# Optimization experiments

Hardware: AMD Instinct MI355X
Metric: run time of the kernel (lower is better)

Reference implementation:

```python
import jax, jax.numpy as jnp
import numpy as np

EPS = 1e-6      # vnn EPS used in norms / leaky-relu denominators
BN_EPS = 1e-5   # torch BatchNorm eps
K = 20          # args.n_knn


def vnlin(W, x):
    # VNLinear: apply (O,C) weight over channel axis 1 of x (B,C,3,...)
    return jnp.moveaxis(jnp.tensordot(W, x, axes=((1,), (1,))), 0, 1)


def vn_bn(x):
    # VNBatchNorm (training-mode batch stats, affine = identity init):
    # normalizes the per-vector norms, rescales vectors accordingly.
    norm = jnp.sqrt(jnp.sum(x * x, axis=2)) + EPS        # (B,C,...)
    axes = (0,) + tuple(range(2, norm.ndim))             # per-channel stats
    mean = jnp.mean(norm, axis=axes, keepdims=True)
    var = jnp.var(norm, axis=axes, keepdims=True)
    norm_bn = (norm - mean) / jnp.sqrt(var + BN_EPS)
    return x / jnp.expand_dims(norm, 2) * jnp.expand_dims(norm_bn, 2)


def vn_lrelu(Wf, Wd, x):
    # VNLinearLeakyReLU with negative_slope=0 (as constructed in this module)
    p = vn_bn(vnlin(Wf, x))
    d = vnlin(Wd, x)
    dot = jnp.sum(p * d, axis=2, keepdims=True)
    dsq = jnp.sum(d * d, axis=2, keepdims=True)
    return jnp.where(dot >= 0, p, p - (dot / (dsq + EPS)) * d)


def vn_maxpool(Wd, x):
    # VNMaxPool: pool over last axis, picking per (b,c) the vector maximizing <x,d>
    d = vnlin(Wd, x)
    dot = jnp.sum(x * d, axis=2, keepdims=True)          # (B,C,1,...)
    idx = jnp.argmax(dot, axis=-1)                       # (B,C,1,...)
    idx = jnp.broadcast_to(idx[..., None], x.shape[:-1] + (1,))
    return jnp.take_along_axis(x, idx, axis=-1)[..., 0]


def graph_feature_cross(x, k):
    # x: (B,3,N) -> (B, 3ch, 3vec, N, k); channels = [nbr-x, x, cross(nbr,x)]
    xx = jnp.sum(x * x, axis=1)                          # (B,N)
    inner = jnp.einsum('bdi,bdj->bij', x, x)             # (B,N,N)
    pd = 2.0 * inner - xx[:, :, None] - xx[:, None, :]   # = -||xi-xj||^2
    idx = jax.lax.top_k(pd, k)[1]                        # (B,N,k) nearest
    pts = jnp.swapaxes(x, 1, 2)                          # (B,N,3)
    nb = jax.vmap(lambda p, i: p[i])(pts, idx)           # (B,N,k,3) gather
    c = jnp.broadcast_to(pts[:, :, None, :], nb.shape)   # center repeated
    cross = jnp.cross(nb, c)
    feat = jnp.stack([nb - c, c, cross], axis=3)         # (B,N,k,3,3)
    return jnp.transpose(feat, (0, 3, 4, 1, 2))


_W_SPECS = {
    'pos_Wf': (21, 3), 'pos_Wd': (21, 3), 'pool_Wd': (21, 21),
    'c1_Wf': (21, 21), 'c1_Wd': (21, 21),
    'st1_Wf': (21, 21), 'st1_Wd': (21, 21),
    'st2_Wf': (42, 21), 'st2_Wd': (42, 21),
    'st3_Wf': (341, 42), 'st3_Wd': (341, 42),
    'st_pool_Wd': (341, 341),
    'stf1_Wf': (170, 341), 'stf1_Wd': (170, 341),
    'stf2_Wf': (85, 170), 'stf2_Wd': (85, 170),
    'stf3_W': (21, 85),
    'c2_Wf': (42, 42), 'c2_Wd': (42, 42),
    'c3_W': (341, 42),
    'std1_Wf': (341, 682), 'std1_Wd': (341, 682),
    'std2_Wf': (170, 341), 'std2_Wd': (170, 341),
    'std_lin': (3, 170),
}


def setup_inputs() -> dict:
    key = jax.random.key(0)
    ks = iter(jax.random.split(key, 32))
    inp = {'x': jax.random.normal(next(ks), (8, 3, 4096), dtype=jnp.float32)}
    for name, (o, i) in _W_SPECS.items():
        inp[name] = jax.random.normal(next(ks), (o, i), dtype=jnp.float32) / np.sqrt(i).astype(np.float32)
    return inp


def _forward(x, pos_Wf, pos_Wd, pool_Wd, c1_Wf, c1_Wd, st1_Wf, st1_Wd, st2_Wf, st2_Wd,
             st3_Wf, st3_Wd, st_pool_Wd, stf1_Wf, stf1_Wd, stf2_Wf, stf2_Wd, stf3_W,
             c2_Wf, c2_Wd, c3_W, std1_Wf, std1_Wd, std2_Wf, std2_Wd, std_lin):
    B, D, N = x.shape
    feat = graph_feature_cross(x, K)                     # (B,3,3,N,k)
    h = vn_lrelu(pos_Wf, pos_Wd, feat)                   # (B,21,3,N,k)
    h = vn_maxpool(pool_Wd, h)                           # (B,21,3,N) pool over k
    h = vn_lrelu(c1_Wf, c1_Wd, h)                        # (B,21,3,N)
    # STNkd feature transform
    s = vn_lrelu(st1_Wf, st1_Wd, h)                      # (B,21,3,N)
    s = vn_lrelu(st2_Wf, st2_Wd, s)                      # (B,42,3,N)
    s = vn_lrelu(st3_Wf, st3_Wd, s)                      # (B,341,3,N)
    s = vn_maxpool(st_pool_Wd, s)                        # (B,341,3) pool over N
    s = vn_lrelu(stf1_Wf, stf1_Wd, s)                    # (B,170,3)
    s = vn_lrelu(stf2_Wf, stf2_Wd, s)                    # (B,85,3)
    s = vnlin(stf3_W, s)                                 # (B,21,3)
    s = jnp.broadcast_to(s[..., None], h.shape)          # repeat over N
    h = jnp.concatenate([h, s], axis=1)                  # (B,42,3,N)
    h = vn_lrelu(c2_Wf, c2_Wd, h)                        # (B,42,3,N)
    h = vn_bn(vnlin(c3_W, h))                            # (B,341,3,N)
    h_mean = jnp.broadcast_to(jnp.mean(h, axis=-1, keepdims=True), h.shape)
    h = jnp.concatenate([h, h_mean], axis=1)             # (B,682,3,N)
    # VNStdFeature (normalize_frame=False)
    z0 = vn_lrelu(std1_Wf, std1_Wd, h)                   # (B,341,3,N)
    z0 = vn_lrelu(std2_Wf, std2_Wd, z0)                  # (B,170,3,N)
    z0 = vnlin(std_lin, z0)                              # (B,3,3,N)
    h_std = jnp.einsum('bijm,bjkm->bikm', h, z0)         # (B,682,3,N)
    out = jnp.max(h_std.reshape(B, -1, N), axis=-1)      # (B,2046)
    return out, z0


def reference(x, pos_Wf, pos_Wd, pool_Wd, c1_Wf, c1_Wd, st1_Wf, st1_Wd, st2_Wf, st2_Wd,
              st3_Wf, st3_Wd, st_pool_Wd, stf1_Wf, stf1_Wd, stf2_Wf, stf2_Wd, stf3_W,
              c2_Wf, c2_Wd, c3_W, std1_Wf, std1_Wd, std2_Wf, std2_Wd, std_lin):
    return _forward(x, pos_Wf, pos_Wd, pool_Wd, c1_Wf, c1_Wd, st1_Wf, st1_Wd, st2_Wf,
                    st2_Wd, st3_Wf, st3_Wd, st_pool_Wd, stf1_Wf, stf1_Wd, stf2_Wf,
                    stf2_Wd, stf3_W, c2_Wf, c2_Wd, c3_W, std1_Wf, std1_Wd, std2_Wf,
                    std2_Wd, std_lin)
```

## Files before the change

kernel.cpp:

```cpp
#include <hip/hip_runtime.h>
#include <cstdint>
#include <cstddef>


typedef unsigned short u16;
using bh8  = __attribute__((ext_vector_type(8))) short;
using f32x4 = __attribute__((ext_vector_type(4))) float;

__device__ __forceinline__ float b2f(u16 v) {
  return __uint_as_float(((unsigned)v) << 16);
}
__device__ __forceinline__ u16 f2b(float f) {
  unsigned u = __float_as_uint(f);
  u += 0x7FFFu + ((u >> 16) & 1u);
  return (u16)(u >> 16);
}

__device__ __forceinline__ void st4(float* p, size_t i, float a, float b, float c, float d) {
  float4 v; v.x = a; v.y = b; v.z = c; v.w = d; *(float4*)(p + i) = v;
}

#define FMA4(A, S, V) { A.x += (S)*(V).x; A.y += (S)*(V).y; A.z += (S)*(V).z; A.w += (S)*(V).w; }

__device__ __forceinline__ unsigned long long packKey(float v, int n) {
// ... 58 lines not shown
  int lane = tid & 63, wave = tid >> 6;
  #pragma unroll
  for (int c = 0; c < 21; ++c) {
    float w0 = wf[c * 3], w1 = wf[c * 3 + 1], w2 = wf[c * 3 + 2];
    float p0 = w0 * e00 + w1 * c0 + w2 * e20;
    float p1 = w0 * e01 + w1 * c1 + w2 * e21;
    float p2 = w0 * e02 + w1 * c2 + w2 * e22;
    float nr = sqrtf(p0 * p0 + p1 * p1 + p2 * p2) + 1e-6f;
    float u1 = nr, u2 = nr * nr;
    #pragma unroll
    for (int off = 32; off; off >>= 1) { u1 += __shfl_down(u1, off); u2 += __shfl_down(u2, off); }
    if (lane == 0) { part[wave][c] = u1; part[wave][21 + c] = u2; }
  }
  __syncthreads();
  if (tid < 42) {
    float t = part[0][tid] + part[1][tid] + part[2][tid] + part[3][tid];
    if (tid < 21) atomicAdd(&statSum[tid], t);
    else atomicAdd(&statSq[tid - 21], t);
  }
}

__global__ __launch_bounds__(64) void pos_apply(const float* __restrict__ x,
                                                const int* __restrict__ idx,
                                                const float* __restrict__ Wf,
                                                const float* __restrict__ Wd,
                                                const float* __restrict__ Wpool,
                                                const float* __restrict__ statMean,
                                                const float* __restrict__ statIstd,
                                                float* __restrict__ h0, int N) {
  __shared__ float wpool[441];
  __shared__ float hbuf[64];
  int tid = threadIdx.x;
  for (int l = tid; l < 441; l += 64) wpool[l] = Wpool[l];
  int b = blockIdx.y, n = blockIdx.x;
  bool act = tid < 63;
  int c = act ? tid / 3 : 0;
  int v = act ? tid - c * 3 : 0;
  const float* xb = x + (size_t)b * 3 * N;
  float c0 = xb[n], c1 = xb[N + n], c2 = xb[2 * (size_t)N + n];
  float wf0 = 0, wf1 = 0, wf2 = 0, wd0 = 0, wd1 = 0, wd2 = 0, mn = 0, is = 1.f;
  if (act) {
    wf0 = Wf[c * 3]; wf1 = Wf[c * 3 + 1]; wf2 = Wf[c * 3 + 2];
    wd0 = Wd[c * 3]; wd1 = Wd[c * 3 + 1]; wd2 = Wd[c * 3 + 2];
    mn = statMean[c]; is = statIstd[c];
  }
  __syncthreads();
  float best = -3.4e38f, bh = 0.f;
  const int* idxRow = idx + ((size_t)b * N + n) * 20;
  for (int kk = 0; kk < 20; ++kk) {
    int j = idxRow[kk];
    float a0 = xb[j], a1 = xb[N + j], a2 = xb[2 * (size_t)N + j];
    float av  = (v == 0) ? a0 : ((v == 1) ? a1 : a2);
    float cv  = (v == 0) ? c0 : ((v == 1) ? c1 : c2);
    float a1v = (v == 0) ? a1 : ((v == 1) ? a2 : a0);
    float a2v = (v == 0) ? a2 : ((v == 1) ? a0 : a1);
    float c1v = (v == 0) ? c1 : ((v == 1) ? c2 : c0);
    float c2v = (v == 0) ? c2 : ((v == 1) ? c0 : c1);
    float e0 = av - cv;
    float e1 = cv;
    float e2 = a1v * c2v - a2v * c1v;
    float p = wf0 * e0 + wf1 * e1 + wf2 * e2;
    float d = wd0 * e0 + wd1 * e1 + wd2 * e2;
    int base = c * 3;
    float pp = p * p;
    float n2 = __shfl(pp, base) + __shfl(pp, base + 1) + __shfl(pp, base + 2);
    float nr = sqrtf(n2) + 1e-6f;
    float sc = ((nr - mn) * is) / nr;
    float pb = p * sc;
    float pd2 = pb * d, dd = d * d;
    float dot = __shfl(pd2, base) + __shfl(pd2, base + 1) + __shfl(pd2, base + 2);
    float dsq = __shfl(dd, base) + __shfl(dd, base + 1) + __shfl(dd, base + 2);
    float h = (dot >= 0.f) ? pb : pb - (dot / (dsq + 1e-6f)) * d;
    hbuf[tid] = act ? h : 0.f;
    __syncthreads();
    float d2 = 0.f;
    #pragma unroll 7
    for (int cc = 0; cc < 21; ++cc) d2 += wpool[c * 21 + cc] * hbuf[cc * 3 + v];
    float hd = h * d2;
    float dotp = __shfl(hd, base) + __shfl(hd, base + 1) + __shfl(hd, base + 2);
    if (act && dotp > best) { best = dotp; bh = h; }
    __syncthreads();
  }
  if (act) h0[(((size_t)b * 32 + c) * 3 + v) * N + n] = bh;
}

__global__ void zero_padch(float* __restrict__ p, int Cfrom, int Cpad, int N) {
  size_t t = (size_t)blockIdx.x * 256 + threadIdx.x;
  size_t per = (size_t)(Cpad - Cfrom) * 3 * N;
  if (t >= 8 * per) return;
  int b = (int)(t / per);
  size_t r = t - (size_t)b * per;
  p[(((size_t)b * Cpad + Cfrom) * 3) * N + r] = 0.f;
}

template<int MODE, int CPT>
__global__ __launch_bounds__(256) void gemm_db(
    const float* __restrict__ Wp, const float* __restrict__ Xp,
    float* __restrict__ Yp,
    float* __restrict__ statSum, float* __restrict__ statSq,
    const float* __restrict__ statMean, const float* __restrict__ statIstd,
    int Cout, int CpadY, int Kpad, int N) {
  __shared__ float Xs[2][16][3][64];
  __shared__ float Wfs[2][16 * CPT][16];
  const int tid = threadIdx.x;
  const int tx = tid & 15, ty = tid >> 4;
  const int lane = tid & 63, w = tid >> 6;
  const int b = blockIdx.z;
  const int n0 = blockIdx.x * 64;
  const int co0 = blockIdx.y * (16 * CPT);
  const float* Xb = Xp + (size_t)b * Kpad * 3 * N;

  auto stage = [&](int k0, int buf) {
    #pragma unroll
    for (int l0 = 0; l0 < 12; ++l0) {
      int q = l0 * 4 + w;
      int vv = q % 3, kk = q / 3;
      const float* g = Xb + ((size_t)(k0 + kk) * 3 + vv) * N + n0 + lane;
      __builtin_amdgcn_global_load_lds(
          (const __attribute__((address_space(1))) float*)g,
          (__attribute__((address_space(3))) float*)&Xs[buf][kk][vv][0], 4, 0, 0);
    }
    #pragma unroll
    for (int c = 0; c < CPT; ++c) {
      const float* g = Wp + (size_t)(co0 + w * 4 + (lane >> 4) + 16 * c) * Kpad + k0 + (lane & 15);
      __builtin_amdgcn_global_load_lds(
          (const __attribute__((address_space(1))) float*)g,
          (__attribute__((address_space(3))) float*)&Wfs[buf][w * 4 + 16 * c][0], 4, 0, 0);
    }
  };

  float4 acc[CPT][3];
  #pragma unroll
  for (int c = 0; c < CPT; ++c)
    #pragma unroll
    for (int v = 0; v < 3; ++v) acc[c][v] = {0.f, 0.f, 0.f, 0.f};

  stage(0, 0);
  __syncthreads();
  const int KT = Kpad / 16;
  for (int kt = 0; kt < KT; ++kt) {
    int buf = kt & 1;
    if (kt + 1 < KT) stage((kt + 1) * 16, buf ^ 1);
    #pragma unroll
    for (int kk = 0; kk < 16; ++kk) {
      float4 x0 = *(const float4*)&Xs[buf][kk][0][tx * 4];
      float4 x1 = *(const float4*)&Xs[buf][kk][1][tx * 4];
      float4 x2 = *(const float4*)&Xs[buf][kk][2][tx * 4];
      #pragma unroll
      for (int c = 0; c < CPT; ++c) {
        float wv = Wfs[buf][ty + 16 * c][kk];
        FMA4(acc[c][0], wv, x0); FMA4(acc[c][1], wv, x1); FMA4(acc[c][2], wv, x2);
      }
    }
    __syncthreads();
  }

  #pragma unroll
  for (int c = 0; c < CPT; ++c) {
    int co = co0 + ty + 16 * c;
    if (co >= CpadY) continue;
    const float* a0 = (const float*)&acc[c][0];
    const float* a1 = (const float*)&acc[c][1];
    const float* a2 = (const float*)&acc[c][2];
    size_t yb = ((size_t)b * CpadY + co) * 3 * N + n0 + tx * 4;
    if constexpr (MODE == 5) {
      float s1 = 0.f, s2 = 0.f;
      #pragma unroll
      for (int j = 0; j < 4; ++j) {
        float nr = sqrtf(a0[j]*a0[j] + a1[j]*a1[j] + a2[j]*a2[j]) + 1e-6f;
        s1 += nr; s2 += nr * nr;
      }
      st4(Yp, yb,                 a0[0], a0[1], a0[2], a0[3]);
      st4(Yp, yb + N,             a1[0], a1[1], a1[2], a1[3]);
      st4(Yp, yb + 2 * (size_t)N, a2[0], a2[1], a2[2], a2[3]);
      #pragma unroll
      for (int off = 8; off; off >>= 1) { s1 += __shfl_down(s1, off); s2 += __shfl_down(s2, off); }
      if (tx == 0 && co < Cout) { atomicAdd(&statSum[co], s1); atomicAdd(&statSq[co], s2); }
    } else {
      if (co < Cout) {
        float mn = statMean[co], is = statIstd[co];
        float4 P0 = *(const float4*)&Yp[yb];
        float4 P1 = *(const float4*)&Yp[yb + N];
        float4 P2 = *(const float4*)&Yp[yb + 2 * (size_t)N];
        float pr[3][4] = {{P0.x,P0.y,P0.z,P0.w},{P1.x,P1.y,P1.z,P1.w},{P2.x,P2.y,P2.z,P2.w}};
        float o_[3][4];
        #pragma unroll
        for (int j = 0; j < 4; ++j) {
          float q0 = pr[0][j], q1 = pr[1][j], q2 = pr[2][j];
          float e0 = a0[j], e1 = a1[j], e2 = a2[j];
          float nr = sqrtf(q0*q0 + q1*q1 + q2*q2) + 1e-6f;
          float sc = ((nr - mn) * is) / nr;
          q0 *= sc; q1 *= sc; q2 *= sc;
          float dot = q0*e0 + q1*e1 + q2*e2;
          if (dot < 0.f) {
            float dsq = e0*e0 + e1*e1 + e2*e2;
            float t = dot / (dsq + 1e-6f);
            q0 -= t*e0; q1 -= t*e1; q2 -= t*e2;
          }
          o_[0][j] = q0; o_[1][j] = q1; o_[2][j] = q2;
        }
        st4(Yp, yb,                 o_[0][0], o_[0][1], o_[0][2], o_[0][3]);
        st4(Yp, yb + N,             o_[1][0], o_[1][1], o_[1][2], o_[1][3]);
        st4(Yp, yb + 2 * (size_t)N, o_[2][0], o_[2][1], o_[2][2], o_[2][3]);
      } else {
        st4(Yp, yb, 0.f, 0.f, 0.f, 0.f);
        st4(Yp, yb + N, 0.f, 0.f, 0.f, 0.f);
        st4(Yp, yb + 2 * (size_t)N, 0.f, 0.f, 0.f, 0.f);
      }
    }
  }
}

__global__ __launch_bounds__(256) void gemm_pool_db(
    const float* __restrict__ Wp, const float* __restrict__ Xp,
    unsigned long long* __restrict__ poolPart, int Cout, int N) {
  constexpr int KP = 352, CPT = 4;
  __shared__ float Xs[2][16][3][64];
  __shared__ float Wfs[2][16 * CPT][16];
  const int tid = threadIdx.x;
  const int tx = tid & 15, ty = tid >> 4;
  const int lane = tid & 63, w = tid >> 6;
  const int b = blockIdx.z;
  const int n0 = blockIdx.x * 64;
  const int co0 = blockIdx.y * (16 * CPT);
  const float* Xb = Xp + (size_t)b * KP * 3 * N;

  auto stage = [&](int k0, int buf) {
    #pragma unroll
    for (int l0 = 0; l0 < 12; ++l0) {
      int q = l0 * 4 + w;
      int vv = q % 3, kk = q / 3;
      const float* g = Xb + ((size_t)(k0 + kk) * 3 + vv) * N + n0 + lane;
      __builtin_amdgcn_global_load_lds(
          (const __attribute__((address_space(1))) float*)g,
          (__attribute__((address_space(3))) float*)&Xs[buf][kk][vv][0], 4, 0, 0);
    }
    #pragma unroll
    for (int c = 0; c < CPT; ++c) {
      const float* g = Wp + (size_t)(co0 + w * 4 + (lane >> 4) + 16 * c) * KP + k0 + (lane & 15);
      __builtin_amdgcn_global_load_lds(
          (const __attribute__((address_space(1))) float*)g,
          (__attribute__((address_space(3))) float*)&Wfs[buf][w * 4 + 16 * c][0], 4, 0, 0);
    }
  };

  float4 acc[CPT][3];
  #pragma unroll
  for (int c = 0; c < CPT; ++c)
    #pragma unroll
    for (int v = 0; v < 3; ++v) acc[c][v] = {0.f, 0.f, 0.f, 0.f};

  stage(0, 0);
  __syncthreads();
  constexpr int KT = KP / 16;
  for (int kt = 0; kt < KT; ++kt) {
    int buf = kt & 1;
    if (kt + 1 < KT) stage((kt + 1) * 16, buf ^ 1);
    #pragma unroll
    for (int kk = 0; kk < 16; ++kk) {
      float4 x0 = *(const float4*)&Xs[buf][kk][0][tx * 4];
      float4 x1 = *(const float4*)&Xs[buf][kk][1][tx * 4];
      float4 x2 = *(const float4*)&Xs[buf][kk][2][tx * 4];
      #pragma unroll
      for (int c = 0; c < CPT; ++c) {
        float wv = Wfs[buf][ty + 16 * c][kk];
        FMA4(acc[c][0], wv, x0); FMA4(acc[c][1], wv, x1); FMA4(acc[c][2], wv, x2);
      }
    }
    __syncthreads();
  }

  #pragma unroll
  for (int c = 0; c < CPT; ++c) {
    int co = co0 + ty + 16 * c;
    unsigned long long key = 0;
    if (co < Cout) {
      const float* av0 = (const float*)&acc[c][0];
      const float* av1 = (const float*)&acc[c][1];
      const float* av2 = (const float*)&acc[c][2];
      size_t xb2 = ((size_t)co * 3) * N + n0 + tx * 4;
      #pragma unroll
      for (int j = 0; j < 4; ++j) {
        float X0 = Xb[xb2 + j];
        float X1 = Xb[xb2 + N + j];
        float X2 = Xb[xb2 + 2 * (size_t)N + j];
        float dot = X0 * av0[j] + X1 * av1[j] + X2 * av2[j];
        unsigned long long k2 = packKey(dot, n0 + tx * 4 + j);
        if (k2 > key) key = k2;
      }
    }
    #pragma unroll
    for (int off = 8; off; off >>= 1) {
      unsigned long long o = __shfl_down(key, off);
      if (o > key) key = o;
    }
    if (tx == 0 && co < Cout) poolPart[((size_t)b * Cout + co) * 64 + blockIdx.x] = key;
  }
}

// ... 35 lines not shown
  for (int s = 0; s < NS; ++s) {
    int cb = co0 + s * 16 + quad * 4;
    if constexpr (MODE == 0) {
      #pragma unroll
      for (int r = 0; r < 4; ++r) {
        int co = cb + r;
        if (co < Cout) {
          size_t zb = (((size_t)b * Cout + co) * 3) * N + n;
          Zout[zb] = acc[s][0][r];
          Zout[zb + N] = acc[s][1][r];
          Zout[zb + 2 * (size_t)N] = acc[s][2][r];
        }
      }
    } else if constexpr (MODE == 1) {
      if (cb < Cpad) {
        float q[3][4];
        #pragma unroll
        for (int r = 0; r < 4; ++r) {
          int co = cb + r;
          float b0 = 0, b1 = 0, b2 = 0;
          if (biasP != nullptr && co < Cout) {
            size_t bi = ((size_t)b * Cout + co) * 3;
            b0 = biasP[bi]; b1 = biasP[bi + 1]; b2 = biasP[bi + 2];
          }
          float q0 = acc[s][0][r] + b0, q1 = acc[s][1][r] + b1, q2 = acc[s][2][r] + b2;
          if (co >= Cout) { q0 = 0.f; q1 = 0.f; q2 = 0.f; }
          q[0][r] = q0; q[1][r] = q1; q[2][r] = q2;
          float nr = sqrtf(q0*q0 + q1*q1 + q2*q2) + 1e-6f;
          float s1 = nr, s2 = nr * nr;
          #pragma unroll
          for (int off = 1; off < 16; off <<= 1) { s1 += __shfl_xor(s1, off); s2 += __shfl_xor(s2, off); }
          if (l16 == 0 && co < Cout) { atomicAdd(&statSum[co], s1); atomicAdd(&statSq[co], s2); }
        }
        #pragma unroll
        for (int v = 0; v < 3; ++v) {
          u16 ob[4];
          ob[0] = f2b(q[v][0]); ob[1] = f2b(q[v][1]); ob[2] = f2b(q[v][2]); ob[3] = f2b(q[v][3]);
          *(ushort4*)(Pb + ((size_t)v * N + n) * Cpad + cb) = *(ushort4*)ob;
        }
      }
    } else {
      if (cb < Cpad) {
        u16 pa[3][4];
        #pragma unroll
        for (int v = 0; v < 3; ++v)
          *(ushort4*)pa[v] = *(const ushort4*)(Pb + ((size_t)v * N + n) * Cpad + cb);
        float o[3][4];
        #pragma unroll
        for (int r = 0; r < 4; ++r) {
          int co = cb + r;
          float r0 = 0.f, r1 = 0.f, r2 = 0.f;
          if (co < Cout) {
            float p0 = b2f(pa[0][r]), p1 = b2f(pa[1][r]), p2 = b2f(pa[2][r]);
            float d0 = acc[s][0][r], d1 = acc[s][1][r], d2 = acc[s][2][r];
            if (biasD != nullptr) {
              size_t bi = ((size_t)b * Cout + co) * 3;
              d0 += biasD[bi]; d1 += biasD[bi + 1]; d2 += biasD[bi + 2];
            }
            float mn = statMean[co], is = statIstd[co];
            float nr = sqrtf(p0*p0 + p1*p1 + p2*p2) + 1e-6f;
            float sc = ((nr - mn) * is) / nr;
            float q0 = p0 * sc, q1 = p1 * sc, q2 = p2 * sc;
            float dot = q0*d0 + q1*d1 + q2*d2;
            if (dot < 0.f) {
              float dsq = d0*d0 + d1*d1 + d2*d2;
              float t = dot / (dsq + 1e-6f);
              q0 -= t*d0; q1 -= t*d1; q2 -= t*d2;
            }
            r0 = q0; r1 = q1; r2 = q2;
          }
          o[0][r] = r0; o[1][r] = r1; o[2][r] = r2;
        }
        #pragma unroll
        for (int v = 0; v < 3; ++v) {
          u16 ob[4];
          ob[0] = f2b(o[v][0]); ob[1] = f2b(o[v][1]); ob[2] = f2b(o[v][2]); ob[3] = f2b(o[v][3]);
          *(ushort4*)(Pb + ((size_t)v * N + n) * Cpad + cb) = *(ushort4*)ob;
        }
      }
    }
  }
}

__global__ void w_to_bf16(const float* __restrict__ W, u16* __restrict__ Wp,
                          int Cout, int Cin, int wstride, int CoutPad, int Kpad) {
  int t = blockIdx.x * 256 + threadIdx.x;
  if (t >= CoutPad * Kpad) return;
  int co = t / Kpad, ci = t - co * Kpad;
  Wp[t] = (co < Cout && ci < Cin) ? f2b(W[(size_t)co * wstride + ci]) : (u16)0;
}

__global__ void w_to_f32pad(const float* __restrict__ W, float* __restrict__ Wp,
                            int Cout, int Cin, int wstride, int CoutPad, int Kpad) {
  int t = blockIdx.x * 256 + threadIdx.x;
  if (t >= CoutPad * Kpad) return;
  int co = t / Kpad, ci = t - co * Kpad;
  Wp[t] = (co < Cout && ci < Cin) ? W[(size_t)co * wstride + ci] : 0.f;
}

__global__ void zero_kernel(float* p, int n) {
  int t = blockIdx.x * 256 + threadIdx.x;
  if (t < n) p[t] = 0.f;
}

__global__ void finalize_kernel(float* __restrict__ sum, float* __restrict__ sq,
                                float* __restrict__ mean, float* __restrict__ istd,
                                int C, float invCount) {
  int c = blockIdx.x * 256 + threadIdx.x;
  if (c < C) {
    float m = sum[c] * invCount;
    float v = sq[c] * invCount - m * m;
    if (v < 0.f) v = 0.f;
    mean[c] = m;
    istd[c] = 1.f / sqrtf(v + 1e-5f);
  }
  if (c < 512) { sum[c] = 0.f; sq[c] = 0.f; }
}

__global__ __launch_bounds__(64) void pool_reduce(const unsigned long long* __restrict__ part,
                                                  const float* __restrict__ s3,
                                                  float* __restrict__ pooled, int N) {
  int co = blockIdx.x, b = blockIdx.y, lane = threadIdx.x;
  unsigned long long key = part[((size_t)b * 341 + co) * 64 + lane];
  #pragma unroll
  for (int off = 32; off; off >>= 1) {
    unsigned long long o = __shfl_down(key, off);
    if (o > key) key = o;
  }
  if (lane == 0) {
    int n = (int)(0xFFFFFFFFu - (unsigned)(key & 0xFFFFFFFFull));
    size_t base = ((size_t)b * 352 + co) * 3;
    size_t obase = ((size_t)b * 341 + co) * 3;
    pooled[obase + 0] = s3[(base + 0) * N + n];
    pooled[obase + 1] = s3[(base + 1) * N + n];
    pooled[obase + 2] = s3[(base + 2) * N + n];
  }
}

__global__ __launch_bounds__(64) void stf_lrelu(const float* __restrict__ Wf,
                                                const float* __restrict__ Wd,
                                                const float* __restrict__ X,
                                                float* __restrict__ Y, int Cin, int Cout) {
  __shared__ float P[24], D[24], NORM[8], SC[8], DOT[8], DSQ[8], MS[2];
  int co = blockIdx.x, tid = threadIdx.x;
  if (tid < 48) {
    int l = tid < 24 ? tid : tid - 24;
    int b = l / 3, v = l - b * 3;
    const float* W = (tid < 24 ? Wf : Wd) + (size_t)co * Cin;
    const float* xb = X + ((size_t)b * Cin) * 3 + v;
    float acc = 0.f;
    for (int ci = 0; ci < Cin; ++ci) acc += W[ci] * xb[ci * 3];
    if (tid < 24) P[l] = acc; else D[l] = acc;
  }
  __syncthreads();
  if (tid < 8) NORM[tid] = sqrtf(P[tid*3]*P[tid*3] + P[tid*3+1]*P[tid*3+1] + P[tid*3+2]*P[tid*3+2]) + 1e-6f;
  __syncthreads();
  if (tid == 0) {
    float m = 0.f;
    for (int b2 = 0; b2 < 8; ++b2) m += NORM[b2];
    m *= 0.125f;
    float var = 0.f;
    for (int b2 = 0; b2 < 8; ++b2) { float dd = NORM[b2] - m; var += dd * dd; }
    var *= 0.125f;
    MS[0] = m; MS[1] = 1.f / sqrtf(var + 1e-5f);
  }
  __syncthreads();
  if (tid < 8) {
    float sc = ((NORM[tid] - MS[0]) * MS[1]) / NORM[tid];
    float dot = 0.f, dsq = 0.f;
    for (int v = 0; v < 3; ++v) {
      float pb = P[tid*3+v] * sc; float dv = D[tid*3+v];
      dot += pb * dv; dsq += dv * dv;
    }
    SC[tid] = sc; DOT[tid] = dot; DSQ[tid] = dsq;
  }
  __syncthreads();
  if (tid < 24) {
    int b = tid / 3;
    float pb = P[tid] * SC[b];
    float o = (DOT[b] >= 0.f) ? pb : pb - (DOT[b] / (DSQ[b] + 1e-6f)) * D[tid];
    Y[((size_t)b * Cout + co) * 3 + (tid - b * 3)] = o;
  }
}

__global__ void vnlin_small(const float* __restrict__ W, const float* __restrict__ X,
                            float* __restrict__ Y, int Cin, int Cout) {
  int t = blockIdx.x * 256 + threadIdx.x;
  if (t >= 8 * Cout * 3) return;
  int v = t % 3, r = t / 3;
  int co = r % Cout, b = r / Cout;
  float acc = 0.f;
  for (int ci = 0; ci < Cin; ++ci) acc += W[(size_t)co * Cin + ci] * X[((size_t)b * Cin + ci) * 3 + v];
  Y[t] = acc;
}

__global__ __launch_bounds__(256) void concat_tt(const float* __restrict__ h1,
                                                 const float* __restrict__ sfin,
                                                 u16* __restrict__ s2bb, int N) {
  __shared__ u16 tile[64][66];
  int b = blockIdx.z, v = blockIdx.y, n0 = blockIdx.x * 64;
  int tn = threadIdx.x & 63, tc = threadIdx.x >> 6;
  for (int c = tc; c < 64; c += 4) {
    u16 val = 0;
    if (c < 21) val = f2b(h1[(((size_t)b * 32 + c) * 3 + v) * N + n0 + tn]);
    else if (c < 42) val = f2b(sfin[((size_t)b * 21 + (c - 21)) * 3 + v]);
    tile[c][tn] = val;
  }
  __syncthreads();
  u16* dst = s2bb + (((size_t)b * 3 + v) * N + n0) * 64;
  for (int n = tc; n < 64; n += 4)
    dst[(size_t)n * 64 + tn] = tile[tn][n];
}

__global__ __launch_bounds__(384) void bn_apply_mean(u16* __restrict__ H,
    const float* __restrict__ sMean, const float* __restrict__ sIstd,
    float* __restrict__ HmAcc, int N) {
  int c = threadIdx.x;
  if (c >= 341) return;
  int b = blockIdx.y, nt = blockIdx.x;
  float mn = sMean[c], is = sIstd[c];
  float a0 = 0.f, a1 = 0.f, a2 = 0.f;
  size_t base = (size_t)b * 3 * N * 352;
  for (int n = nt * 64; n < nt * 64 + 64; ++n) {
    size_t i0 = base + ((size_t)0 * N + n) * 352 + c;
    size_t i1 = base + ((size_t)1 * N + n) * 352 + c;
    size_t i2 = base + ((size_t)2 * N + n) * 352 + c;
    float p0 = b2f(H[i0]), p1 = b2f(H[i1]), p2 = b2f(H[i2]);
    float nr = sqrtf(p0*p0 + p1*p1 + p2*p2) + 1e-6f;
    float sc = ((nr - mn) * is) / nr;
    p0 *= sc; p1 *= sc; p2 *= sc;
    H[i0] = f2b(p0); H[i1] = f2b(p1); H[i2] = f2b(p2);
    a0 += p0; a1 += p1; a2 += p2;
  }
  size_t hb = ((size_t)b * 341 + c) * 3;
  atomicAdd(&HmAcc[hb], a0); atomicAdd(&HmAcc[hb + 1], a1); atomicAdd(&HmAcc[hb + 2], a2);
}

__global__ void hm_finalize(float* Hm, float invN) {
  int t = blockIdx.x * 256 + threadIdx.x;
  if (t < 8 * 341 * 3) Hm[t] *= invN;
}

__global__ void bias_kernel(const float* __restrict__ Wf, const float* __restrict__ Wd,
                            const float* __restrict__ Hm,
                            float* __restrict__ biasP, float* __restrict__ biasD) {
  int t = blockIdx.x * 256 + threadIdx.x;
  if (t >= 8 * 341 * 3) return;
  int v = t % 3, r = t / 3;
  int co = r % 341, b = r / 341;
  const float* hm = Hm + (size_t)b * 1023 + v;
  float ap = 0.f, ad = 0.f;
  for (int j = 0; j < 341; ++j) {
    float h = hm[j * 3];
    ap += Wf[(size_t)co * 682 + 341 + j] * h;
    ad += Wd[(size_t)co * 682 + 341 + j] * h;
  }
  biasP[t] = ap; biasD[t] = ad;
}

__global__ __launch_bounds__(256) void final_max_part(const u16* __restrict__ H,
    const float* __restrict__ Hm, const float* __restrict__ z0,
    float* __restrict__ part, int N, int NT) {
  __shared__ float red[3][4][64];
  int b = blockIdx.z, nt = blockIdx.y;
  int il = threadIdx.x & 63, nsub = threadIdx.x >> 6;
  int i = blockIdx.x * 64 + il;
  bool valid = i < 682, lo = i < 341;
  float c0 = 0, c1 = 0, c2 = 0;
  if (valid && !lo) {
    size_t hb = ((size_t)b * 341 + (i - 341)) * 3;
    c0 = Hm[hb]; c1 = Hm[hb + 1]; c2 = Hm[hb + 2];
  }
  const float* zb = z0 + (size_t)b * 9 * N;
  const u16* Hb = H + (size_t)b * 3 * N * 352;
  float m0 = -3.4e38f, m1 = -3.4e38f, m2 = -3.4e38f;
  int ii = lo ? i : 0;
  int chunk = N / NT, nBeg = nt * chunk;
  for (int n = nBeg + nsub; n < nBeg + chunk; n += 4) {
    float a0, a1, a2;
    if (lo) {
      a0 = b2f(Hb[((size_t)0 * N + n) * 352 + ii]);
      a1 = b2f(Hb[((size_t)1 * N + n) * 352 + ii]);
      a2 = b2f(Hb[((size_t)2 * N + n) * 352 + ii]);
    } else { a0 = c0; a1 = c1; a2 = c2; }
    float s0 = a0 * zb[n]                + a1 * zb[3 * (size_t)N + n] + a2 * zb[6 * (size_t)N + n];
    float s1 = a0 * zb[N + n]            + a1 * zb[4 * (size_t)N + n] + a2 * zb[7 * (size_t)N + n];
    float s2 = a0 * zb[2 * (size_t)N + n]+ a1 * zb[5 * (size_t)N + n] + a2 * zb[8 * (size_t)N + n];
    m0 = fmaxf(m0, s0); m1 = fmaxf(m1, s1); m2 = fmaxf(m2, s2);
  }
  red[0][nsub][il] = m0; red[1][nsub][il] = m1; red[2][nsub][il] = m2;
  __syncthreads();
  if (nsub == 0 && valid) {
    for (int q = 1; q < 4; ++q) {
      m0 = fmaxf(m0, red[0][q][il]); m1 = fmaxf(m1, red[1][q][il]); m2 = fmaxf(m2, red[2][q][il]);
    }
    size_t pb = ((size_t)b * 682 + i) * 3;
    part[(pb + 0) * NT + nt] = m0;
    part[(pb + 1) * NT + nt] = m1;
    part[(pb + 2) * NT + nt] = m2;
  }
}

__global__ void final_max_reduce(const float* __restrict__ part,
                                 float* __restrict__ out, int NT) {
  int t = blockIdx.x * 256 + threadIdx.x;
  if (t >= 8 * 682 * 3) return;
  const float* p = part + (size_t)t * NT;
  float m = p[0];
  for (int k = 1; k < NT; ++k) m = fmaxf(m, p[k]);
  out[t] = m;
}

extern "C" void kernel_launch(void* const* d_in, const int* in_sizes, int n_in,
                              void* d_out, int out_size, void* d_ws, size_t ws_size,
                              hipStream_t stream) {
  (void)in_sizes; (void)n_in; (void)out_size; (void)ws_size;
  const float* x       = (const float*)d_in[0];
  const float* pos_Wf  = (const float*)d_in[1];
  const float* pos_Wd  = (const float*)d_in[2];
  const float* pool_Wd = (const float*)d_in[3];
  const float* c1_Wf   = (const float*)d_in[4];
  const float* c1_Wd   = (const float*)d_in[5];
  const float* st1_Wf  = (const float*)d_in[6];
  const float* st1_Wd  = (const float*)d_in[7];
  const float* st2_Wf  = (const float*)d_in[8];
  const float* st2_Wd  = (const float*)d_in[9];
  const float* st3_Wf  = (const float*)d_in[10];
  const float* st3_Wd  = (const float*)d_in[11];
  const float* stp_Wd  = (const float*)d_in[12];
  const float* stf1_Wf = (const float*)d_in[13];
  const float* stf1_Wd = (const float*)d_in[14];
  const float* stf2_Wf = (const float*)d_in[15];
  const float* stf2_Wd = (const float*)d_in[16];
  const float* stf3_W  = (const float*)d_in[17];
  const float* c2_Wf   = (const float*)d_in[18];
  const float* c2_Wd   = (const float*)d_in[19];
  const float* c3_W    = (const float*)d_in[20];
  const float* std1_Wf = (const float*)d_in[21];
  const float* std1_Wd = (const float*)d_in[22];
  const float* std2_Wf = (const float*)d_in[23];
  const float* std2_Wd = (const float*)d_in[24];
  const float* stdlin  = (const float*)d_in[25];

  float* outv  = (float*)d_out;
  float* z0out = outv + 8 * 2046;

  const int N = 4096;
  const int NT = 32;
  char* ws = (char*)d_ws;
  size_t off = 0;
  auto alloc = [&](size_t bytes) -> char* {
    char* p = ws + off;
    off += (bytes + 255) & ~(size_t)255;
    return p;
  };
  float* stats = (float*)alloc(2048 * sizeof(float));
  float* sSum = stats, *sSq = stats + 512, *sMean = stats + 1024, *sIstd = stats + 1536;
  int* idx = (int*)alloc((size_t)8 * N * 20 * 4);
  unsigned long long* poolPart = (unsigned long long*)alloc((size_t)8 * 341 * 64 * 8);
  float* fmPart = (float*)alloc((size_t)8 * 682 * 3 * NT * 4);
  float* Wpoolp = (float*)alloc((size_t)384 * 352 * 4);
  float* Wc1f = (float*)alloc(32 * 32 * 4);
  float* Wc1d = (float*)alloc(32 * 32 * 4);
  float* Ws1f = (float*)alloc(32 * 32 * 4);
  float* Ws1d = (float*)alloc(32 * 32 * 4);
  float* Ws2f = (float*)alloc(64 * 32 * 4);
  float* Ws2d = (float*)alloc(64 * 32 * 4);
  float* Ws3f = (float*)alloc(352 * 48 * 4);
  float* Ws3d = (float*)alloc(352 * 48 * 4);
  float* pooled = (float*)alloc(8 * 341 * 3 * 4);
  float* stf1o  = (float*)alloc(8 * 170 * 3 * 4);
  float* stf2o  = (float*)alloc(8 * 85 * 3 * 4);
  float* sfin   = (float*)alloc(8 * 21 * 3 * 4);
  float* Hm     = (float*)alloc(8 * 1023 * 4);
  float* biasP  = (float*)alloc(8 * 341 * 3 * 4);
  float* biasD  = (float*)alloc(8 * 341 * 3 * 4);
  const size_t P32 = (size_t)8 * 32 * 3 * N;
  const size_t P48 = (size_t)8 * 48 * 3 * N;
  const size_t T352 = (size_t)8 * 3 * N * 352 * 2;
  const size_t T192 = (size_t)8 * 3 * N * 192 * 2;
  const size_t T64  = (size_t)8 * 3 * N * 64 * 2;
  const size_t F352 = (size_t)8 * 352 * 3 * N * 4;
  char* regionA = alloc(T352);
  char* regionB = alloc(F352);
  float* h0  = (float*)regionA;
  float* h1  = h0 + P32;
  float* s1b = h1 + P32;
  float* s2b = s1b + P32;
  float* st3o = (float*)regionB;
  u16* Hbuf  = (u16*)regionB;
  u16* Pstd2 = (u16*)(regionB + T352);
  u16* s2bb  = (u16*)(regionB + T352 + T192);
  u16* h2b   = (u16*)(regionB + T352 + T192 + T64);
  u16* Pstd1 = (u16*)regionA;
  u16* W1fp = (u16*)poolPart;
  u16* W1dp = W1fp + 384 * 352;
  u16* W2fp = W1dp + 384 * 352;
  u16* W2dp = W2fp + 192 * 352;
  u16* Wc3p = W2dp + 192 * 352;
  u16* Wc2f = Wc3p + 384 * 64;
  u16* Wc2d = Wc2f + 64 * 64;
  u16* Wzp  = Wc2d + 64 * 64;

  dim3 blk256(256), blk64(64);
  const float invBN = 1.f / (8.f * N);
  auto run_db = [&](const float* Wfp, const float* Wdp, const float* X, float* Y,
                    int Cout, int CpadY, int Kpad, int coTiles, float invCnt) {
    dim3 grid(64, coTiles, 8);
    gemm_db<5, 2><<<grid, blk256, 0, stream>>>(Wfp, X, Y, sSum, sSq, nullptr, nullptr,
                                               Cout, CpadY, Kpad, N);
    finalize_kernel<<<dim3(2), blk256, 0, stream>>>(sSum, sSq, sMean, sIstd, Cout, invCnt);
    gemm_db<6, 2><<<grid, blk256, 0, stream>>>(Wdp, X, Y, nullptr, nullptr, sMean, sIstd,
                                               Cout, CpadY, Kpad, N);
  };
  auto run_mfma = [&](const u16* Wf, const u16* Wd, const u16* X, u16* P,
                      const float* bP, const float* bD,
                      int Cout, int Cpad, int Kpad, int coTiles) {
    dim3 grid(64, coTiles, 8);
    mfma2<1, 4><<<grid, blk256, 0, stream>>>(Wf, X, P, nullptr, bP, nullptr,
                                             sSum, sSq, nullptr, nullptr, Cout, Cpad, Kpad, N);
    finalize_kernel<<<dim3(2), blk256, 0, stream>>>(sSum, sSq, sMean, sIstd, Cout, invBN);
    mfma2<2, 4><<<grid, blk256, 0, stream>>>(Wd, X, P, nullptr, nullptr, bD,
                                             nullptr, nullptr, sMean, sIstd, Cout, Cpad, Kpad, N);
  };

  zero_kernel<<<dim3(4), blk256, 0, stream>>>(stats, 1024);
  w_to_f32pad<<<dim3((384 * 352 + 255) / 256), blk256, 0, stream>>>(stp_Wd, Wpoolp, 341, 341, 341, 384, 352);
  w_to_f32pad<<<dim3((32 * 32 + 255) / 256), blk256, 0, stream>>>(c1_Wf, Wc1f, 21, 21, 21, 32, 32);
  w_to_f32pad<<<dim3((32 * 32 + 255) / 256), blk256, 0, stream>>>(c1_Wd, Wc1d, 21, 21, 21, 32, 32);
  w_to_f32pad<<<dim3((32 * 32 + 255) / 256), blk256, 0, stream>>>(st1_Wf, Ws1f, 21, 21, 21, 32, 32);
  w_to_f32pad<<<dim3((32 * 32 + 255) / 256), blk256, 0, stream>>>(st1_Wd, Ws1d, 21, 21, 21, 32, 32);
  w_to_f32pad<<<dim3((64 * 32 + 255) / 256), blk256, 0, stream>>>(st2_Wf, Ws2f, 42, 21, 21, 64, 32);
  w_to_f32pad<<<dim3((64 * 32 + 255) / 256), blk256, 0, stream>>>(st2_Wd, Ws2d, 42, 21, 21, 64, 32);
  w_to_f32pad<<<dim3((352 * 48 + 255) / 256), blk256, 0, stream>>>(st3_Wf, Ws3f, 341, 42, 42, 352, 48);
  w_to_f32pad<<<dim3((352 * 48 + 255) / 256), blk256, 0, stream>>>(st3_Wd, Ws3d, 341, 42, 42, 352, 48);
  zero_padch<<<dim3((8 * 11 * 3 * N + 255) / 256), blk256, 0, stream>>>(h0, 21, 32, N);

  knn_kernel<<<dim3(N / 4, 8), blk256, 0, stream>>>(x, idx, N);
  pos_stats<<<dim3(N * 20 / 256, 8), blk256, 0, stream>>>(x, idx, pos_Wf, sSum, sSq, N);
  finalize_kernel<<<dim3(2), blk256, 0, stream>>>(sSum, sSq, sMean, sIstd, 21, 1.f / (8.f * N * 20.f));
  pos_apply<<<dim3(N, 8), blk64, 0, stream>>>(x, idx, pos_Wf, pos_Wd, pool_Wd, sMean, sIstd, h0, N);

  run_db(Wc1f, Wc1d, h0, h1, 21, 32, 32, 1, invBN);
  run_db(Ws1f, Ws1d, h1, s1b, 21, 32, 32, 1, invBN);
  run_db(Ws2f, Ws2d, s1b, s2b, 42, 48, 32, 2, invBN);
  run_db(Ws3f, Ws3d, s2b, st3o, 341, 352, 48, 11, invBN);

  gemm_pool_db<<<dim3(64, 6, 8), blk256, 0, stream>>>(Wpoolp, st3o, poolPart, 341, N);
  pool_reduce<<<dim3(341, 8), blk64, 0, stream>>>(poolPart, st3o, pooled, N);

  w_to_bf16<<<dim3((384 * 352 + 255) / 256), blk256, 0, stream>>>(std1_Wf, W1fp, 341, 341, 682, 384, 352);
  w_to_bf16<<<dim3((384 * 352 + 255) / 256), blk256, 0, stream>>>(std1_Wd, W1dp, 341, 341, 682, 384, 352);
  w_to_bf16<<<dim3((192 * 352 + 255) / 256), blk256, 0, stream>>>(std2_Wf, W2fp, 170, 341, 341, 192, 352);
  w_to_bf16<<<dim3((192 * 352 + 255) / 256), blk256, 0, stream>>>(std2_Wd, W2dp, 170, 341, 341, 192, 352);
  w_to_bf16<<<dim3((384 * 64 + 255) / 256), blk256, 0, stream>>>(c3_W, Wc3p, 341, 42, 42, 384, 64);
  w_to_bf16<<<dim3((64 * 64 + 255) / 256), blk256, 0, stream>>>(c2_Wf, Wc2f, 42, 42, 42, 64, 64);
  w_to_bf16<<<dim3((64 * 64 + 255) / 256), blk256, 0, stream>>>(c2_Wd, Wc2d, 42, 42, 42, 64, 64);
  w_to_bf16<<<dim3((16 * 192 + 255) / 256), blk256, 0, stream>>>(stdlin, Wzp, 3, 170, 170, 16, 192);

  stf_lrelu<<<dim3(170), blk64, 0, stream>>>(stf1_Wf, stf1_Wd, pooled, stf1o, 341, 170);
  stf_lrelu<<<dim3(85),  blk64, 0, stream>>>(stf2_Wf, stf2_Wd, stf1o, stf2o, 170, 85);
  vnlin_small<<<dim3(2), blk256, 0, stream>>>(stf3_W, stf2o, sfin, 85, 21);

  concat_tt<<<dim3(N / 64, 3, 8), blk256, 0, stream>>>(h1, sfin, s2bb, N);
  run_mfma(Wc2f, Wc2d, s2bb, h2b, nullptr, nullptr, 42, 64, 64, 1);

  {
    dim3 grid(64, 6, 8);
    mfma2<1, 4><<<grid, blk256, 0, stream>>>(Wc3p, h2b, Hbuf, nullptr, nullptr, nullptr,
                                             sSum, sSq, nullptr, nullptr, 341, 352, 64, N);
  }
  finalize_kernel<<<dim3(2), blk256, 0, stream>>>(sSum, sSq, sMean, sIstd, 341, invBN);
  zero_kernel<<<dim3(32), blk256, 0, stream>>>(Hm, 8 * 1023);
  bn_apply_mean<<<dim3(64, 8), dim3(384), 0, stream>>>(Hbuf, sMean, sIstd, Hm, N);
  hm_finalize<<<dim3(32), blk256, 0, stream>>>(Hm, 1.f / (float)N);
  bias_kernel<<<dim3(32), blk256, 0, stream>>>(std1_Wf, std1_Wd, Hm, biasP, biasD);

  run_mfma(W1fp, W1dp, Hbuf, Pstd1, biasP, biasD, 341, 352, 352, 6);
  run_mfma(W2fp, W2dp, Pstd1, Pstd2, nullptr, nullptr, 170, 192, 352, 3);

  mfma2<0, 1><<<dim3(64, 1, 8), blk256, 0, stream>>>(Wzp, Pstd2, nullptr, z0out,
                                                     nullptr, nullptr, nullptr, nullptr,
                                                     nullptr, nullptr, 3, 16, 192, N);
  final_max_part<<<dim3(11, NT, 8), blk256, 0, stream>>>(Hbuf, Hm, z0out, fmPart, N, NT);
  final_max_reduce<<<dim3((8 * 682 * 3 + 255) / 256), blk256, 0, stream>>>(fmPart, outv, NT);
}
```

Measured before the change: 2.684 ms.

## Batch weight-padding launches, fold hm_finalize, and widen CPT for st3 and pool GEMMs

Merges the many small weight-padding, zeroing and bf16-conversion kernels into two combined prep kernels. The separate mean-scaling kernel is removed by passing 1/N into bias_kernel and final_max_part. The st3 GEMMs and the pool GEMM now use larger output-channel tiles (CPT 4 and 6) with fewer blocks. Together these cut launch count and per-block overhead, at the cost of less parallelism in the wider-tile GEMMs.

Result: faster. 2.614 ms (-2.6%).

```diff
diff --git a/kernel.cpp b/kernel.cpp
--- a/kernel.cpp
+++ b/kernel.cpp
@@ -164,15 +164,6 @@
     __syncthreads();
   }
   if (act) h0[(((size_t)b * 32 + c) * 3 + v) * N + n] = bh;
-}
-
-__global__ void zero_padch(float* __restrict__ p, int Cfrom, int Cpad, int N) {
-  size_t t = (size_t)blockIdx.x * 256 + threadIdx.x;
-  size_t per = (size_t)(Cpad - Cfrom) * 3 * N;
-  if (t >= 8 * per) return;
-  int b = (int)(t / per);
-  size_t r = t - (size_t)b * per;
-  p[(((size_t)b * Cpad + Cfrom) * 3) * N + r] = 0.f;
 }
 
 template<int MODE, int CPT>
@@ -296,7 +287,7 @@
 __global__ __launch_bounds__(256) void gemm_pool_db(
     const float* __restrict__ Wp, const float* __restrict__ Xp,
     unsigned long long* __restrict__ poolPart, int Cout, int N) {
-  constexpr int KP = 352, CPT = 4;
+  constexpr int KP = 352, CPT = 6;
   __shared__ float Xs[2][16][3][64];
   __shared__ float Wfs[2][16 * CPT][16];
   const int tid = threadIdx.x;
@@ -498,20 +489,73 @@
   }
 }
 
-__global__ void w_to_bf16(const float* __restrict__ W, u16* __restrict__ Wp,
-                          int Cout, int Cin, int wstride, int CoutPad, int Kpad) {
-  int t = blockIdx.x * 256 + threadIdx.x;
-  if (t >= CoutPad * Kpad) return;
-  int co = t / Kpad, ci = t - co * Kpad;
-  Wp[t] = (co < Cout && ci < Cin) ? f2b(W[(size_t)co * wstride + ci]) : (u16)0;
-}
-
-__global__ void w_to_f32pad(const float* __restrict__ W, float* __restrict__ Wp,
-                            int Cout, int Cin, int wstride, int CoutPad, int Kpad) {
-  int t = blockIdx.x * 256 + threadIdx.x;
-  if (t >= CoutPad * Kpad) return;
-  int co = t / Kpad, ci = t - co * Kpad;
-  Wp[t] = (co < Cout && ci < Cin) ? W[(size_t)co * wstride + ci] : 0.f;
+__device__ __forceinline__ void padf32(size_t r, const float* W, float* Wp,
+                                       int Cout, int Cin, int ws, int Kpad) {
+  int co = (int)(r / Kpad), ci = (int)(r - (size_t)co * Kpad);
+  Wp[r] = (co < Cout && ci < Cin) ? W[(size_t)co * ws + ci] : 0.f;
+}
+__global__ void prep_f32(float* stats,
+                         const float* stpW, float* Wpoolp,
+                         const float* c1f, float* Wc1f, const float* c1d, float* Wc1d,
+                         const float* s1f, float* Ws1f, const float* s1d, float* Ws1d,
+                         const float* s2f, float* Ws2f, const float* s2d, float* Ws2d,
+                         const float* s3f, float* Ws3f, const float* s3d, float* Ws3d,
+                         float* h0, int N) {
+  size_t t = (size_t)blockIdx.x * 256 + threadIdx.x;
+  if (t < 1024) { stats[t] = 0.f; return; }
+  t -= 1024;
+  if (t < 135168) { padf32(t, stpW, Wpoolp, 341, 341, 341, 352); return; }
+  t -= 135168;
+  if (t < 1024) { padf32(t, c1f, Wc1f, 21, 21, 21, 32); return; }
+  t -= 1024;
+  if (t < 1024) { padf32(t, c1d, Wc1d, 21, 21, 21, 32); return; }
+  t -= 1024;
+  if (t < 1024) { padf32(t, s1f, Ws1f, 21, 21, 21, 32); return; }
+  t -= 1024;
+  if (t < 1024) { padf32(t, s1d, Ws1d, 21, 21, 21, 32); return; }
+  t -= 1024;
+  if (t < 2048) { padf32(t, s2f, Ws2f, 42, 21, 21, 32); return; }
+  t -= 2048;
+  if (t < 2048) { padf32(t, s2d, Ws2d, 42, 21, 21, 32); return; }
+  t -= 2048;
+  if (t < 18432) { padf32(t, s3f, Ws3f, 341, 42, 42, 48); return; }
+  t -= 18432;
+  if (t < 18432) { padf32(t, s3d, Ws3d, 341, 42, 42, 48); return; }
+  t -= 18432;
+  size_t per = (size_t)11 * 3 * N;
+  if (t < 8 * per) {
+    int b = (int)(t / per);
+    size_t r = t - (size_t)b * per;
+    h0[(((size_t)b * 32 + 21) * 3) * N + r] = 0.f;
+  }
+}
+
+__device__ __forceinline__ void padbf(size_t r, const float* W, u16* Wp,
+                                      int Cout, int Cin, int ws, int Kpad) {
+  int co = (int)(r / Kpad), ci = (int)(r - (size_t)co * Kpad);
+  Wp[r] = (co < Cout && ci < Cin) ? f2b(W[(size_t)co * ws + ci]) : (u16)0;
+}
+__global__ void prep_bf16(const float* w1f, u16* W1fp, const float* w1d, u16* W1dp,
+                          const float* w2f, u16* W2fp, const float* w2d, u16* W2dp,
+                          const float* c3w, u16* Wc3p,
+                          const float* c2f, u16* Wc2f, const float* c2d, u16* Wc2d,
+                          const float* zl, u16* Wzp) {
+  size_t t = (size_t)blockIdx.x * 256 + threadIdx.x;
+  if (t < 135168) { padbf(t, w1f, W1fp, 341, 341, 682, 352); return; }
+  t -= 135168;
+  if (t < 135168) { padbf(t, w1d, W1dp, 341, 341, 682, 352); return; }
+  t -= 135168;
+  if (t < 67584) { padbf(t, w2f, W2fp, 170, 341, 341, 352); return; }
+  t -= 67584;
+  if (t < 67584) { padbf(t, w2d, W2dp, 170, 341, 341, 352); return; }
+  t -= 67584;
+  if (t < 24576) { padbf(t, c3w, Wc3p, 341, 42, 42, 64); return; }
+  t -= 24576;
+  if (t < 4096) { padbf(t, c2f, Wc2f, 42, 42, 42, 64); return; }
+  t -= 4096;
+  if (t < 4096) { padbf(t, c2d, Wc2d, 42, 42, 42, 64); return; }
+  t -= 4096;
+  if (t < 3072) { padbf(t, zl, Wzp, 3, 170, 170, 192); }
 }
 
 __global__ void zero_kernel(float* p, int n) {
@@ -652,13 +696,8 @@
   atomicAdd(&HmAcc[hb], a0); atomicAdd(&HmAcc[hb + 1], a1); atomicAdd(&HmAcc[hb + 2], a2);
 }
 
-__global__ void hm_finalize(float* Hm, float invN) {
-  int t = blockIdx.x * 256 + threadIdx.x;
-  if (t < 8 * 341 * 3) Hm[t] *= invN;
-}
-
 __global__ void bias_kernel(const float* __restrict__ Wf, const float* __restrict__ Wd,
-                            const float* __restrict__ Hm,
+                            const float* __restrict__ Hm, float invN,
                             float* __restrict__ biasP, float* __restrict__ biasD) {
   int t = blockIdx.x * 256 + threadIdx.x;
   if (t >= 8 * 341 * 3) return;
@@ -667,7 +706,7 @@
   const float* hm = Hm + (size_t)b * 1023 + v;
   float ap = 0.f, ad = 0.f;
   for (int j = 0; j < 341; ++j) {
-    float h = hm[j * 3];
+    float h = hm[j * 3] * invN;
     ap += Wf[(size_t)co * 682 + 341 + j] * h;
     ad += Wd[(size_t)co * 682 + 341 + j] * h;
   }
@@ -675,7 +714,7 @@
 }
 
 __global__ __launch_bounds__(256) void final_max_part(const u16* __restrict__ H,
-    const float* __restrict__ Hm, const float* __restrict__ z0,
+    const float* __restrict__ Hm, float invN, const float* __restrict__ z0,
     float* __restrict__ part, int N, int NT) {
   __shared__ float red[3][4][64];
   int b = blockIdx.z, nt = blockIdx.y;
@@ -685,7 +724,7 @@
   float c0 = 0, c1 = 0, c2 = 0;
   if (valid && !lo) {
     size_t hb = ((size_t)b * 341 + (i - 341)) * 3;
-    c0 = Hm[hb]; c1 = Hm[hb + 1]; c2 = Hm[hb + 2];
+    c0 = Hm[hb] * invN; c1 = Hm[hb + 1] * invN; c2 = Hm[hb + 2] * invN;
   }
   const float* zb = z0 + (size_t)b * 9 * N;
   const u16* Hb = H + (size_t)b * 3 * N * 352;
@@ -782,8 +821,8 @@
   float* Ws1d = (float*)alloc(32 * 32 * 4);
   float* Ws2f = (float*)alloc(64 * 32 * 4);
   float* Ws2d = (float*)alloc(64 * 32 * 4);
-  float* Ws3f = (float*)alloc(352 * 48 * 4);
-  float* Ws3d = (float*)alloc(352 * 48 * 4);
+  float* Ws3f = (float*)alloc(384 * 48 * 4);
+  float* Ws3d = (float*)alloc(384 * 48 * 4);
   float* pooled = (float*)alloc(8 * 341 * 3 * 4);
   float* stf1o  = (float*)alloc(8 * 170 * 3 * 4);
   float* stf2o  = (float*)alloc(8 * 85 * 3 * 4);
@@ -792,7 +831,6 @@
   float* biasP  = (float*)alloc(8 * 341 * 3 * 4);
   float* biasD  = (float*)alloc(8 * 341 * 3 * 4);
   const size_t P32 = (size_t)8 * 32 * 3 * N;
-  const size_t P48 = (size_t)8 * 48 * 3 * N;
   const size_t T352 = (size_t)8 * 3 * N * 352 * 2;
   const size_t T192 = (size_t)8 * 3 * N * 192 * 2;
   const size_t T64  = (size_t)8 * 3 * N * 64 * 2;
@@ -820,15 +858,6 @@
 
   dim3 blk256(256), blk64(64);
   const float invBN = 1.f / (8.f * N);
-  auto run_db = [&](const float* Wfp, const float* Wdp, const float* X, float* Y,
-                    int Cout, int CpadY, int Kpad, int coTiles, float invCnt) {
-    dim3 grid(64, coTiles, 8);
-    gemm_db<5, 2><<<grid, blk256, 0, stream>>>(Wfp, X, Y, sSum, sSq, nullptr, nullptr,
-                                               Cout, CpadY, Kpad, N);
-    finalize_kernel<<<dim3(2), blk256, 0, stream>>>(sSum, sSq, sMean, sIstd, Cout, invCnt);
-    gemm_db<6, 2><<<grid, blk256, 0, stream>>>(Wdp, X, Y, nullptr, nullptr, sMean, sIstd,
-                                               Cout, CpadY, Kpad, N);
-  };
   auto run_mfma = [&](const u16* Wf, const u16* Wd, const u16* X, u16* P,
                       const float* bP, const float* bD,
                       int Cout, int Cpad, int Kpad, int coTiles) {
@@ -840,39 +869,41 @@
                                              nullptr, nullptr, sMean, sIstd, Cout, Cpad, Kpad, N);
   };
 
-  zero_kernel<<<dim3(4), blk256, 0, stream>>>(stats, 1024);
-  w_to_f32pad<<<dim3((384 * 352 + 255) / 256), blk256, 0, stream>>>(stp_Wd, Wpoolp, 341, 341, 341, 384, 352);
-  w_to_f32pad<<<dim3((32 * 32 + 255) / 256), blk256, 0, stream>>>(c1_Wf, Wc1f, 21, 21, 21, 32, 32);
-  w_to_f32pad<<<dim3((32 * 32 + 255) / 256), blk256, 0, stream>>>(c1_Wd, Wc1d, 21, 21, 21, 32, 32);
-  w_to_f32pad<<<dim3((32 * 32 + 255) / 256), blk256, 0, stream>>>(st1_Wf, Ws1f, 21, 21, 21, 32, 32);
-  w_to_f32pad<<<dim3((32 * 32 + 255) / 256), blk256, 0, stream>>>(st1_Wd, Ws1d, 21, 21, 21, 32, 32);
-  w_to_f32pad<<<dim3((64 * 32 + 255) / 256), blk256, 0, stream>>>(st2_Wf, Ws2f, 42, 21, 21, 64, 32);
-  w_to_f32pad<<<dim3((64 * 32 + 255) / 256), blk256, 0, stream>>>(st2_Wd, Ws2d, 42, 21, 21, 64, 32);
-  w_to_f32pad<<<dim3((352 * 48 + 255) / 256), blk256, 0, stream>>>(st3_Wf, Ws3f, 341, 42, 42, 352, 48);
-  w_to_f32pad<<<dim3((352 * 48 + 255) / 256), blk256, 0, stream>>>(st3_Wd, Ws3d, 341, 42, 42, 352, 48);
-  zero_padch<<<dim3((8 * 11 * 3 * N + 255) / 256), blk256, 0, stream>>>(h0, 21, 32, N);
-
+  {
+    size_t tot = 1024 + 135168 + 4 * 1024 + 2 * 2048 + 2 * 18432 + (size_t)8 * 11 * 3 * N;
+    prep_f32<<<dim3((unsigned)((tot + 255) / 256)), blk256, 0, stream>>>(
+        stats, stp_Wd, Wpoolp, c1_Wf, Wc1f, c1_Wd, Wc1d, st1_Wf, Ws1f, st1_Wd, Ws1d,
+        st2_Wf, Ws2f, st2_Wd, Ws2d, st3_Wf, Ws3f, st3_Wd, Ws3d, h0, N);
+  }
   knn_kernel<<<dim3(N / 4, 8), blk256, 0, stream>>>(x, idx, N);
   pos_stats<<<dim3(N * 20 / 256, 8), blk256, 0, stream>>>(x, idx, pos_Wf, sSum, sSq, N);
   finalize_kernel<<<dim3(2), blk256, 0, stream>>>(sSum, sSq, sMean, sIstd, 21, 1.f / (8.f * N * 20.f));
   pos_apply<<<dim3(N, 8), blk64, 0, stream>>>(x, idx, pos_Wf, pos_Wd, pool_Wd, sMean, sIstd, h0, N);
 
-  run_db(Wc1f, Wc1d, h0, h1, 21, 32, 32, 1, invBN);
-  run_db(Ws1f, Ws1d, h1, s1b, 21, 32, 32, 1, invBN);
-  run_db(Ws2f, Ws2d, s1b, s2b, 42, 48, 32, 2, invBN);
-  run_db(Ws3f, Ws3d, s2b, st3o, 341, 352, 48, 11, invBN);
-
-  gemm_pool_db<<<dim3(64, 6, 8), blk256, 0, stream>>>(Wpoolp, st3o, poolPart, 341, N);
+  {
+    dim3 g1(64, 1, 8);
+    gemm_db<5, 2><<<g1, blk256, 0, stream>>>(Wc1f, h0, h1, sSum, sSq, nullptr, nullptr, 21, 32, 32, N);
+    finalize_kernel<<<dim3(2), blk256, 0, stream>>>(sSum, sSq, sMean, sIstd, 21, invBN);
+    gemm_db<6, 2><<<g1, blk256, 0, stream>>>(Wc1d, h0, h1, nullptr, nullptr, sMean, sIstd, 21, 32, 32, N);
+    gemm_db<5, 2><<<g1, blk256, 0, stream>>>(Ws1f, h1, s1b, sSum, sSq, nullptr, nullptr, 21, 32, 32, N);
+    finalize_kernel<<<dim3(2), blk256, 0, stream>>>(sSum, sSq, sMean, sIstd, 21, invBN);
+    gemm_db<6, 2><<<g1, blk256, 0, stream>>>(Ws1d, h1, s1b, nullptr, nullptr, sMean, sIstd, 21, 32, 32, N);
+    dim3 g2(64, 2, 8);
+    gemm_db<5, 2><<<g2, blk256, 0, stream>>>(Ws2f, s1b, s2b, sSum, sSq, nullptr, nullptr, 42, 48, 32, N);
+    finalize_kernel<<<dim3(2), blk256, 0, stream>>>(sSum, sSq, sMean, sIstd, 42, invBN);
+    gemm_db<6, 2><<<g2, blk256, 0, stream>>>(Ws2d, s1b, s2b, nullptr, nullptr, sMean, sIstd, 42, 48, 32, N);
+    dim3 g3(64, 6, 8);
+    gemm_db<5, 4><<<g3, blk256, 0, stream>>>(Ws3f, s2b, st3o, sSum, sSq, nullptr, nullptr, 341, 352, 48, N);
+    finalize_kernel<<<dim3(2), blk256, 0, stream>>>(sSum, sSq, sMean, sIstd, 341, invBN);
+    gemm_db<6, 4><<<g3, blk256, 0, stream>>>(Ws3d, s2b, st3o, nullptr, nullptr, sMean, sIstd, 341, 352, 48, N);
+  }
+
+  gemm_pool_db<<<dim3(64, 4, 8), blk256, 0, stream>>>(Wpoolp, st3o, poolPart, 341, N);
   pool_reduce<<<dim3(341, 8), blk64, 0, stream>>>(poolPart, st3o, pooled, N);
 
-  w_to_bf16<<<dim3((384 * 352 + 255) / 256), blk256, 0, stream>>>(std1_Wf, W1fp, 341, 341, 682, 384, 352);
-  w_to_bf16<<<dim3((384 * 352 + 255) / 256), blk256, 0, stream>>>(std1_Wd, W1dp, 341, 341, 682, 384, 352);
-  w_to_bf16<<<dim3((192 * 352 + 255) / 256), blk256, 0, stream>>>(std2_Wf, W2fp, 170, 341, 341, 192, 352);
-  w_to_bf16<<<dim3((192 * 352 + 255) / 256), blk256, 0, stream>>>(std2_Wd, W2dp, 170, 341, 341, 192, 352);
-  w_to_bf16<<<dim3((384 * 64 + 255) / 256), blk256, 0, stream>>>(c3_W, Wc3p, 341, 42, 42, 384, 64);
-  w_to_bf16<<<dim3((64 * 64 + 255) / 256), blk256, 0, stream>>>(c2_Wf, Wc2f, 42, 42, 42, 64, 64);
-  w_to_bf16<<<dim3((64 * 64 + 255) / 256), blk256, 0, stream>>>(c2_Wd, Wc2d, 42, 42, 42, 64, 64);
-  w_to_bf16<<<dim3((16 * 192 + 255) / 256), blk256, 0, stream>>>(stdlin, Wzp, 3, 170, 170, 16, 192);
+  prep_bf16<<<dim3((441344 + 255) / 256), blk256, 0, stream>>>(
+      std1_Wf, W1fp, std1_Wd, W1dp, std2_Wf, W2fp, std2_Wd, W2dp,
+      c3_W, Wc3p, c2_Wf, Wc2f, c2_Wd, Wc2d, stdlin, Wzp);
 
   stf_lrelu<<<dim3(170), blk64, 0, stream>>>(stf1_Wf, stf1_Wd, pooled, stf1o, 341, 170);
   stf_lrelu<<<dim3(85),  blk64, 0, stream>>>(stf2_Wf, stf2_Wd, stf1o, stf2o, 170, 85);
@@ -889,8 +920,7 @@
   finalize_kernel<<<dim3(2), blk256, 0, stream>>>(sSum, sSq, sMean, sIstd, 341, invBN);
   zero_kernel<<<dim3(32), blk256, 0, stream>>>(Hm, 8 * 1023);
   bn_apply_mean<<<dim3(64, 8), dim3(384), 0, stream>>>(Hbuf, sMean, sIstd, Hm, N);
-  hm_finalize<<<dim3(32), blk256, 0, stream>>>(Hm, 1.f / (float)N);
-  bias_kernel<<<dim3(32), blk256, 0, stream>>>(std1_Wf, std1_Wd, Hm, biasP, biasD);
+  bias_kernel<<<dim3(32), blk256, 0, stream>>>(std1_Wf, std1_Wd, Hm, 1.f / (float)N, biasP, biasD);
 
   run_mfma(W1fp, W1dp, Hbuf, Pstd1, biasP, biasD, 341, 352, 352, 6);
   run_mfma(W2fp, W2dp, Pstd1, Pstd2, nullptr, nullptr, 170, 192, 352, 3);
@@ -898,6 +928,6 @@
   mfma2<0, 1><<<dim3(64, 1, 8), blk256, 0, stream>>>(Wzp, Pstd2, nullptr, z0out,
                                                      nullptr, nullptr, nullptr, nullptr,
                                                      nullptr, nullptr, 3, 16, 192, N);
-  final_max_part<<<dim3(11, NT, 8), blk256, 0, stream>>>(Hbuf, Hm, z0out, fmPart, N, NT);
+  final_max_part<<<dim3(11, NT, 8), blk256, 0, stream>>>(Hbuf, Hm, 1.f / (float)N, z0out, fmPart, N, NT);
   final_max_reduce<<<dim3((8 * 682 * 3 + 255) / 256), blk256, 0, stream>>>(fmPart, outv, NT);
 }
```
